# Performance work log

Measured on AMD Instinct MI355X. Metric: run time of the kernel, lower is better.

The kernel has to match this reference:

```python
import jax, jax.numpy as jnp
import numpy as np

B, M, GRID = 4, 8192, 32          # batches, points per batch, voxel grid side
N = B * M
K = 8                              # knn neighbors (includes self at dist 0)
C_IN, C_OUT, H = 8, 8, 128
KEYB = 64                          # hash base (coords shifted +1 stay in [0,33])
EPS = 1e-5


def setup_inputs() -> dict:
    rng = np.random.default_rng(0)
    # unique occupied voxels per batch (ME SparseTensor requires unique coords)
    cs = []
    for b in range(B):
        lin = rng.choice(GRID ** 3, size=M, replace=False)
        x, y, z = lin // (GRID * GRID), (lin // GRID) % GRID, lin % GRID
        cs.append(np.stack([np.full(M, b), x, y, z], axis=1))
    coords = jnp.asarray(np.concatenate(cs, axis=0).astype(np.int32))  # [N,4]

    key = jax.random.key(0)
    ks = jax.random.split(key, 4)
    feats = jax.random.normal(ks[0], (N, C_IN), jnp.float32)
    w1 = jax.random.normal(ks[1], ((K + 1) * C_IN, H), jnp.float32) * 0.05  # 1x1 conv
    g1 = jnp.ones((H,), jnp.float32)
    b1 = jnp.zeros((H,), jnp.float32)
    w3 = jax.random.normal(ks[2], (27, H, H), jnp.float32) * 0.02          # 3^3 sparse conv
    g2 = jnp.ones((H,), jnp.float32)
    b2 = jnp.zeros((H,), jnp.float32)
    w_out = jax.random.normal(ks[3], (H, 2 * C_OUT), jnp.float32) * 0.05   # 1x1 conv
    return dict(coords=coords, feats=feats, w1=w1, g1=g1, b1=b1,
                w3=w3, g2=g2, b2=b2, w_out=w_out)


def _knn_idx(coords):
    # per-batch brute-force kNN on xyz (batch column segments the search)
    xyz = coords[:, 1:].astype(jnp.float32).reshape(B, M, 3)
    d2 = jnp.sum((xyz[:, :, None, :] - xyz[:, None, :, :]) ** 2, -1)  # [B,M,M]
    _, idx = jax.lax.top_k(-d2, K)                                     # [B,M,K]
    return (idx + (jnp.arange(B) * M)[:, None, None]).reshape(N, K)


def _bn(x, g, b):
    mu = jnp.mean(x, axis=0)
    var = jnp.var(x, axis=0)
    return (x - mu) * jax.lax.rsqrt(var + EPS) * g + b


def reference(coords, feats, w1, g1, b1, w3, g2, b2, w_out):
    # --- kNN gather-and-build: [center || k neighbor feats] -> (k+1)*C_in ---
    nbr = _knn_idx(coords)                                        # [N,K] int
    combined = jnp.concatenate([feats[:, None, :], feats[nbr]], axis=1)
    combined = combined.reshape(N, (K + 1) * C_IN)
    # --- neighbor_processor: 1x1 conv + BN + ReLU ---
    h = jax.nn.relu(_bn(combined @ w1, g1, b1))                   # [N,H]
    # --- context_predictor conv k=3: gather inputs at coord+offset via hash ---
    c = coords[:, 1:] + 1                                         # shift so offsets stay >= 0
    keys = ((coords[:, 0] * KEYB + c[:, 0]) * KEYB + c[:, 1]) * KEYB + c[:, 2]
    order = jnp.argsort(keys)
    skeys = keys[order]
    offs = jnp.stack(jnp.meshgrid(*([jnp.arange(-1, 2)] * 3), indexing='ij'),
                     axis=-1).reshape(27, 3)                      # {-1,0,1}^3
    okey = (offs[:, 0] * KEYB + offs[:, 1]) * KEYB + offs[:, 2]   # [27]
    q = keys[None, :] + okey[:, None]                             # [27,N]
    pos = jnp.clip(jnp.searchsorted(skeys, q), 0, N - 1)
    valid = skeys[pos] == q                                       # [27,N]
    j = order[pos]                                                # [27,N]
    gathered = jnp.where(valid[..., None], h[j], 0.0)             # [27,N,H]
    h2 = jnp.einsum('onc,ocd->nd', gathered, w3)                  # [N,H]
    h2 = jax.nn.relu(_bn(h2, g2, b2))
    # --- final 1x1 conv -> mean/scale ---
    return h2 @ w_out                                             # [N, 2*C_OUT]
```

## Files before the change

kernel.cpp:

```cpp
#include <hip/hip_runtime.h>
#include <hip/hip_bf16.h>

#define B_   4
#define M_   8192
#define N_   32768
#define H_   128
#define EPS_ 1e-5f
#define TBL  1048576
#define GUARD 8192

typedef short short8 __attribute__((ext_vector_type(8)));
typedef float f32x4  __attribute__((ext_vector_type(4)));

__global__ __launch_bounds__(256) void prep_pack_kernel(const int* __restrict__ coords,
                                                        int* __restrict__ table,
                                                        int* __restrict__ packed,
                                                        int* __restrict__ keyb,
                                                        const float* __restrict__ w3,
                                                        ushort* __restrict__ w3f,
                                                        float* __restrict__ gsum1,
                                                        float* __restrict__ gsum2,
                                                        unsigned int* __restrict__ hbz) {
    int bid = blockIdx.x, tid = threadIdx.x;
    if (bid < 128) {
        int n = bid * 256 + tid;
        int b = coords[4*n+0], x = coords[4*n+1], y = coords[4*n+2], z = coords[4*n+3];
        packed[n] = (x << 10) | (y << 5) | z;
        int key = ((b*64 + x+1)*64 + y+1)*64 + (z+1);
        keyb[n] = key;
        table[key] = n;
        if (bid < 8)  gsum1[bid*256 + tid] = 0.f;
        if (bid == 0) gsum2[tid] = 0.f;
        if (bid == 8 && tid < 64) hbz[tid] = 0u;
        return;
    }
    int t = (bid - 128) * 256 + tid;
    int lane = t & 63;
    int ct   = (t >> 6) & 7;
    int ks   = (t >> 9) & 3;
    int o    = t >> 11;
    int quad = lane >> 4, l15 = lane & 15;
    int n = ct*16 + l15;
    const float* src = w3 + o*16384;
    ushort out8[8];
#pragma unroll
    for (int j = 0; j < 8; ++j) {
        int c = ks*32 + quad*8 + j;
        float v = src[c*128 + n];
        __hip_bfloat16 bv = __float2bfloat16(v);
        ushort u; __builtin_memcpy(&u, &bv, 2);
        out8[j] = u;
    }
    *(uint4*)&w3f[t*8] = *(uint4*)out8;
}

__global__ __launch_bounds__(256) void knn_kernel(const int* __restrict__ table,
                                                  const int* __restrict__ keyb,
                                                  const int* __restrict__ packed,
                                                  int* __restrict__ nbr) {
    __shared__ int okey_sh[96], d2_sh[96];
    __shared__ int tops[256 * 8];
    __shared__ int flagq[64];
    __shared__ int ncnt, fln;
    int tid = threadIdx.x;
    if (tid == 0) { ncnt = 0; fln = 0; }
    __syncthreads();
    if (tid < 125) {
        int dx = tid / 25 - 2, rr = tid % 25, dy = rr / 5 - 2, dz = rr % 5 - 2;
        int d2 = dx*dx + dy*dy + dz*dz;
        if (d2 <= 8) {
            int p = atomicAdd(&ncnt, 1);
            okey_sh[p] = dx * 4096 + dy * 64 + dz;
            d2_sh[p]   = d2;
        }
    }
    __syncthreads();
    if (tid < 3) { okey_sh[93 + tid] = 0; d2_sh[93 + tid] = 9; }
    __syncthreads();

    int q   = blockIdx.x * 64 + (tid >> 2);
    int sub = tid & 3;
    int kb  = keyb[q];

    int jv[24];
    int base = sub * 24;
#pragma unroll
    for (int i = 0; i < 24; ++i)
        jv[i] = table[kb + okey_sh[base + i]];

    int top[8];
#pragma unroll
    for (int k = 0; k < 8; ++k) top[k] = 0x7FFFFFFF;
#pragma unroll
    for (int i = 0; i < 24; ++i) {
        int j = jv[i];
        if (j >= 0) {
            int key = (d2_sh[base + i] << 13) | (j & 8191);
            if (key < top[7]) {
#pragma unroll
                for (int k = 7; k >= 1; --k)
                    top[k] = (key < top[k]) ? max(key, top[k-1]) : top[k];
                top[0] = min(key, top[0]);
            }
        }
    }
#pragma unroll
    for (int k = 0; k < 8; ++k) tops[tid*8 + k] = top[k];
    __syncthreads();

    if (sub == 0) {
        const int* L = &tops[tid*8];
        int ia0 = 0, ia1 = 0, ia2 = 0, ia3 = 0;
        int res[8];
#pragma unroll
        for (int k = 0; k < 8; ++k) {
            int v0 = L[ia0], v1 = L[8 + ia1], v2 = L[16 + ia2], v3 = L[24 + ia3];
            int m01 = min(v0, v1), m23 = min(v2, v3);
            int m = min(m01, m23);
            res[k] = m;
            if (m == v0) ++ia0; else if (m == v1) ++ia1;
            else if (m == v2) ++ia2; else ++ia3;
        }
        int bb = q & ~(M_-1);
        if ((res[7] >> 13) <= 8) {
#pragma unroll
            for (int k = 0; k < 8; ++k) nbr[q*8 + k] = bb + (res[k] & 8191);
        } else {
            int pos = atomicAdd(&fln, 1);
            flagq[pos] = q;
        }
    }
    __syncthreads();

    int cnt = fln;
    for (int f = 0; f < cnt; ++f) {
        int n = flagq[f];
        int bb = n & ~(M_-1);
        int p = packed[n];
        int qx = (p >> 10) & 31, qy = (p >> 5) & 31, qz = p & 31;
        int bt[8];
#pragma unroll
        for (int k = 0; k < 8; ++k) bt[k] = 0x7FFFFFFF;
        for (int j = tid; j < M_; j += 256) {
            int c = packed[bb + j];
            int dx = qx - ((c >> 10) & 31);
            int dy = qy - ((c >> 5) & 31);
            int dz = qz - (c & 31);
            int d2 = dx*dx + dy*dy + dz*dz;
            int key = (d2 << 13) | j;
            if (key < bt[7]) {
#pragma unroll
                for (int k = 7; k >= 1; --k)
                    bt[k] = (key < bt[k]) ? max(key, bt[k-1]) : bt[k];
                bt[0] = min(key, bt[0]);
            }
        }
#pragma unroll
        for (int k = 0; k < 8; ++k) tops[tid*8 + k] = bt[k];
        __syncthreads();
        for (int stride = 128; stride >= 1; stride >>= 1) {
            if (tid < stride) {
                int* A  = &tops[tid*8];
                int* Bp = &tops[(tid+stride)*8];
                int r[8]; int ia = 0, ib = 0;
#pragma unroll
                for (int k = 0; k < 8; ++k) {
                    int a = A[ia], b2 = Bp[ib];
                    if (a <= b2) { r[k] = a; ++ia; } else { r[k] = b2; ++ib; }
                }
#pragma unroll
                for (int k = 0; k < 8; ++k) A[k] = r[k];
            }
            __syncthreads();
        }
        if (tid == 0) {
#pragma unroll
            for (int k = 0; k < 8; ++k) nbr[n*8 + k] = bb + (tops[k] & 8191);
        }
        __syncthreads();
    }
}

__global__ __launch_bounds__(256) void h1_kernel(const float* __restrict__ feats,
                                                 const int* __restrict__ nbr,
                                                 const float* __restrict__ w1,
                                                 float* __restrict__ hpre,
                                                 float* __restrict__ gsum1) {
    __shared__ float comb[16][72];
    __shared__ float ssum[256], ssq[256];
    int tid = threadIdx.x;
    int rowbase = blockIdx.x * 16;
    if (tid < 144) {
        int r = tid / 9, s = tid % 9;
        int grow = rowbase + r;
        int idx = (s == 0) ? grow : nbr[grow*8 + (s-1)];
        const float4* f = (const float4*)(feats + idx * 8);
        float4 a = f[0], b = f[1];
        float* dp = &comb[r][s*8];
        dp[0]=a.x; dp[1]=a.y; dp[2]=a.z; dp[3]=a.w;
        dp[4]=b.x; dp[5]=b.y; dp[6]=b.z; dp[7]=b.w;
    }
    __syncthreads();
    int c = tid & 127, rh = tid >> 7;
    float acc[8];
#pragma unroll
    for (int i = 0; i < 8; ++i) acc[i] = 0.f;
    for (int s = 0; s < 72; ++s) {
        float w = w1[s*128 + c];
#pragma unroll
        for (int i = 0; i < 8; ++i)
            acc[i] += comb[rh*8 + i][s] * w;
    }
    float s = 0.f, q = 0.f;
#pragma unroll
    for (int i = 0; i < 8; ++i) {
        hpre[(rowbase + rh*8 + i)*128 + c] = acc[i];
        s += acc[i]; q += acc[i]*acc[i];
    }
    ssum[tid] = s; ssq[tid] = q;
    __syncthreads();
    if (tid < 128) {
        float S = ssum[tid] + ssum[tid+128];
        float Q = ssq[tid]  + ssq[tid+128];
        float* g = gsum1 + (blockIdx.x & 7) * 256;
        atomicAdd(&g[tid], S);
        atomicAdd(&g[128 + tid], Q);
    }
}

__global__ __launch_bounds__(256) void bnrelu_bf16_kernel(const float* __restrict__ x,
                                                          const float* __restrict__ gsum1,
                                                          const float* __restrict__ g1,
                                                          const float* __restrict__ b1,
                                                          ushort* __restrict__ y) {
    __shared__ float sc[128], sh[128];
    int tid = threadIdx.x;
    if (tid < 128) {
        float s = 0.f, q = 0.f;
#pragma unroll
        for (int r = 0; r < 8; ++r) {
            s += gsum1[r*256 + tid];
            q += gsum1[r*256 + 128 + tid];
        }
        float mu  = s / (float)N_;
        float var = q / (float)N_ - mu*mu;
        float inv = rsqrtf(var + EPS_);
        float scv = inv * g1[tid];
        sc[tid] = scv;
        sh[tid] = b1[tid] - mu * scv;
    }
    __syncthreads();
    int i = blockIdx.x * 256 + tid;
    float4 v = ((const float4*)x)[i];
    int c = (i * 4) & 127;
    v.x = fmaxf(0.f, v.x*sc[c]   + sh[c]);
    v.y = fmaxf(0.f, v.y*sc[c+1] + sh[c+1]);
    v.z = fmaxf(0.f, v.z*sc[c+2] + sh[c+2]);
    v.w = fmaxf(0.f, v.w*sc[c+3] + sh[c+3]);
    ushort o[4];
#pragma unroll
    for (int k = 0; k < 4; ++k) {
        float f = (&v.x)[k];
        __hip_bfloat16 bv = __float2bfloat16(f);
        __builtin_memcpy(&o[k], &bv, 2);
    }
    ((ushort4*)y)[i] = make_ushort4(o[0], o[1], o[2], o[3]);
}

#define CONV3_LDS 145408
__global__ __launch_bounds__(512) void conv3_mfma_kernel(const ushort* __restrict__ hb,
                                                         const ushort* __restrict__ w3f,
                                                         const int* __restrict__ table,
                                                         const int* __restrict__ keyb,
                                                         float* __restrict__ h2,
                                                         float* __restrict__ gsum) {
    extern __shared__ char smem_raw[];
    ushort* Asb = (ushort*)smem_raw;
    ushort* Bsb = (ushort*)(smem_raw + 65536);
    int*    jsh = (int*)(smem_raw + 131072);
    int*    kbsh= (int*)(smem_raw + 144896);

    int tid = threadIdx.x;
    int lane = tid & 63, wid = tid >> 6;
    int quad = lane >> 4, l15 = lane & 15;
    int bid = blockIdx.x;
    int swz = (bid & 7) * 32 + (bid >> 3);
    int rowbase = swz * 128;
    int wr = wid >> 1;
    int cb = (wid & 1) * 4;

    if (tid < 128) kbsh[tid] = keyb[rowbase + tid];
    __syncthreads();
    for (int t = tid; t < 27*128; t += 512) {
        int o = t >> 7, r = t & 127;
        int dx = o/9 - 1, dy = (o/3)%3 - 1, dz = o%3 - 1;
        jsh[t] = table[kbsh[r] + dx*4096 + dy*64 + dz];
    }
    __syncthreads();

#pragma unroll
    for (int i = 0; i < 4; ++i) {
        int flat = i*512 + tid;
        int r = flat >> 4, cp = flat & 15;
        int j = jsh[r];
        const ushort* asrc = hb + j*128 + ((cp ^ (r & 15)) << 3);
        __builtin_amdgcn_global_load_lds(
            (const __attribute__((address_space(1))) unsigned int*)asrc,
            (__attribute__((address_space(3))) unsigned int*)&Asb[flat << 3],
            16, 0, 0);
        __builtin_amdgcn_global_load_lds(
            (const __attribute__((address_space(1))) unsigned int*)(w3f + (flat << 3)),
            (__attribute__((address_space(3))) unsigned int*)&Bsb[flat << 3],
            16, 0, 0);
    }
    __syncthreads();

    f32x4 acc[2][4];
#pragma unroll
    for (int i = 0; i < 2; ++i)
#pragma unroll
        for (int c = 0; c < 4; ++c)
            acc[i][c] = (f32x4){0.f, 0.f, 0.f, 0.f};

    int cur = 0;
#pragma unroll 1
    for (int o = 0; o < 27; ++o) {
        if (o < 26) {
            int obase = (o + 1) << 7;
            const ushort* wsrc = w3f + ((o + 1) << 14);
            int dst = (cur ^ 1) * 16384;
#pragma unroll
            for (int i = 0; i < 4; ++i) {
                int flat = i*512 + tid;
                int r = flat >> 4, cp = flat & 15;
                int j = jsh[obase + r];
                const ushort* asrc = hb + j*128 + ((cp ^ (r & 15)) << 3);
                __builtin_amdgcn_global_load_lds(
                    (const __attribute__((address_space(1))) unsigned int*)asrc,
                    (__attribute__((address_space(3))) unsigned int*)&Asb[dst + (flat << 3)],
                    16, 0, 0);
                __builtin_amdgcn_global_load_lds(
                    (const __attribute__((address_space(1))) unsigned int*)(wsrc + (flat << 3)),
                    (__attribute__((address_space(3))) unsigned int*)&Bsb[dst + (flat << 3)],
                    16, 0, 0);
            }
        }
        const ushort* Ac = Asb + cur*16384;
        const ushort* Bc = Bsb + cur*16384;
#pragma unroll
        for (int ks = 0; ks < 4; ++ks) {
            short8 af[2], bfr[4];
#pragma unroll
            for (int i = 0; i < 2; ++i) {
                int lr = wr*32 + i*16 + l15;
                int chunk = (ks*4 + quad) ^ l15;
                af[i] = *(const short8*)&Ac[lr*128 + chunk*8];
            }
#pragma unroll
            for (int c = 0; c < 4; ++c)
                bfr[c] = *(const short8*)&Bc[((ks*8 + cb + c)*64 + lane) << 3];
#pragma unroll
            for (int i = 0; i < 2; ++i)
#pragma unroll
                for (int c = 0; c < 4; ++c)
                    acc[i][c] = __builtin_amdgcn_mfma_f32_16x16x32_bf16(af[i], bfr[c], acc[i][c], 0, 0, 0);
        }
        __syncthreads();
        cur ^= 1;
    }

    float s[4], q[4];
#pragma unroll
    for (int c = 0; c < 4; ++c) { s[c] = 0.f; q[c] = 0.f; }
#pragma unroll
    for (int i = 0; i < 2; ++i)
#pragma unroll
        for (int c = 0; c < 4; ++c)
#pragma unroll
            for (int r = 0; r < 4; ++r) {
                int row = rowbase + wr*32 + i*16 + quad*4 + r;
                int col = (cb + c)*16 + l15;
                float v = acc[i][c][r];
                h2[row*128 + col] = v;
                s[c] += v; q[c] += v*v;
            }
    float* red = (float*)smem_raw;
    if (tid < 256) red[tid] = 0.f;
    __syncthreads();
#pragma unroll
    for (int c = 0; c < 4; ++c) {
        int col = (cb + c)*16 + l15;
        atomicAdd(&red[col], s[c]);
        atomicAdd(&red[128 + col], q[c]);
    }
    __syncthreads();
    if (tid < 256) atomicAdd(&gsum[tid], red[tid]);
}

__global__ __launch_bounds__(256) void out_kernel(const float* __restrict__ h2,
                                                  const float* __restrict__ wout,
                                                  const float* __restrict__ gsum2,
                                                  const float* __restrict__ g2,
                                                  const float* __restrict__ b2,
                                                  float* __restrict__ out) {
    __shared__ float hrow[128][129];
    __shared__ float wsh[2048];
    __shared__ float sc[128], sh[128];
    int tid = threadIdx.x;
    if (tid < 128) {
        float s = gsum2[tid], q = gsum2[128 + tid];
        float mu  = s / (float)N_;
        float var = q / (float)N_ - mu*mu;
        float inv = rsqrtf(var + EPS_);
        float scv = inv * g2[tid];
        sc[tid] = scv;
        sh[tid] = b2[tid] - mu * scv;
    }
#pragma unroll
    for (int i = 0; i < 8; ++i) wsh[i*256 + tid] = wout[i*256 + tid];
    __syncthreads();

    int rowbase = blockIdx.x * 128;
#pragma unroll
    for (int i = 0; i < 16; ++i) {
        int flat = i*256 + tid;
        int row = flat >> 5, c4 = (flat & 31) * 4;
        float4 v = *(const float4*)&h2[(rowbase + row)*128 + c4];
        float4 scv = *(const float4*)&sc[c4];
        float4 shv = *(const float4*)&sh[c4];
        hrow[row][c4+0] = fmaxf(0.f, fmaf(v.x, scv.x, shv.x));
        hrow[row][c4+1] = fmaxf(0.f, fmaf(v.y, scv.y, shv.y));
        hrow[row][c4+2] = fmaxf(0.f, fmaf(v.z, scv.z, shv.z));
        hrow[row][c4+3] = fmaxf(0.f, fmaf(v.w, scv.w, shv.w));
    }
    __syncthreads();

    int row = tid >> 1, dbase = (tid & 1) * 8;
    float acc[8];
#pragma unroll
    for (int k = 0; k < 8; ++k) acc[k] = 0.f;
    for (int c = 0; c < 128; ++c) {
        float hv = hrow[row][c];
        float4 w0 = *(const float4*)&wsh[c*16 + dbase];
        float4 w1 = *(const float4*)&wsh[c*16 + dbase + 4];
        acc[0] = fmaf(hv, w0.x, acc[0]);
        acc[1] = fmaf(hv, w0.y, acc[1]);
        acc[2] = fmaf(hv, w0.z, acc[2]);
        acc[3] = fmaf(hv, w0.w, acc[3]);
        acc[4] = fmaf(hv, w1.x, acc[4]);
        acc[5] = fmaf(hv, w1.y, acc[5]);
        acc[6] = fmaf(hv, w1.z, acc[6]);
        acc[7] = fmaf(hv, w1.w, acc[7]);
    }
    float* op = out + (rowbase + row)*16 + dbase;
    *(float4*)op       = (float4){acc[0], acc[1], acc[2], acc[3]};
    *(float4*)(op + 4) = (float4){acc[4], acc[5], acc[6], acc[7]};
}

extern "C" void kernel_launch(void* const* d_in, const int* in_sizes, int n_in,
                              void* d_out, int out_size, void* d_ws, size_t ws_size,
                              hipStream_t stream) {
    const int*   coords = (const int*)d_in[0];
    const float* feats  = (const float*)d_in[1];
    const float* w1     = (const float*)d_in[2];
    const float* g1     = (const float*)d_in[3];
    const float* b1     = (const float*)d_in[4];
    const float* w3     = (const float*)d_in[5];
    const float* g2     = (const float*)d_in[6];
    const float* b2     = (const float*)d_in[7];
    const float* wout   = (const float*)d_in[8];
    float* out = (float*)d_out;

    char* ws = (char*)d_ws;
    int*    table_base = (int*)(ws);
    int*    table   = table_base + GUARD;
    int*    packed  = (int*)(ws + (4352u<<10));
    int*    keyb    = (int*)(ws + (4608u<<10));
    int*    nbr     = (int*)(ws + (4864u<<10));
    float*  gsum2   = (float*)(ws + (6416u<<10));
    float*  gsum1   = (float*)(ws + (6420u<<10));
    ushort* w3f     = (ushort*)(ws + (6656u<<10));
    ushort* hb      = (ushort*)(ws + (7680u<<10));
    float*  h       = (float*)(ws + (15872u<<10));
    float*  h2      = h;

    static bool conv3_attr_set = false;
    if (!conv3_attr_set) {
        hipFuncSetAttribute(reinterpret_cast<const void*>(&conv3_mfma_kernel),
                            hipFuncAttributeMaxDynamicSharedMemorySize, CONV3_LDS);
        conv3_attr_set = true;
    }

    hipMemsetAsync(table_base, 0xFF, (TBL + GUARD) * sizeof(int), stream);
    prep_pack_kernel <<<344, 256, 0, stream>>>(coords, table, packed, keyb, w3, w3f,
                                               gsum1, gsum2, (unsigned int*)(hb - 128));
    knn_kernel       <<<N_/64, 256, 0, stream>>>(table, keyb, packed, nbr);
    h1_kernel        <<<N_/16, 256, 0, stream>>>(feats, nbr, w1, h, gsum1);
    bnrelu_bf16_kernel<<<(N_*H_/4)/256, 256, 0, stream>>>(h, gsum1, g1, b1, hb);
    conv3_mfma_kernel<<<N_/128, 512, CONV3_LDS, stream>>>(hb, w3f, table, keyb, h2, gsum2);
    out_kernel       <<<N_/128, 256, 0, stream>>>(h2, wout, gsum2, g2, b2, out);
}
```

Before: 220.8 us.

## Fuse kNN search with first 1x1 conv, keep neighbor indices in LDS

```diff
diff --git a/kernel.cpp b/kernel.cpp
--- a/kernel.cpp
+++ b/kernel.cpp
@@ -54,14 +54,20 @@
     *(uint4*)&w3f[t*8] = *(uint4*)out8;
 }
 
-__global__ __launch_bounds__(256) void knn_kernel(const int* __restrict__ table,
-                                                  const int* __restrict__ keyb,
-                                                  const int* __restrict__ packed,
-                                                  int* __restrict__ nbr) {
-    __shared__ int okey_sh[96], d2_sh[96];
+__global__ __launch_bounds__(256) void knn_h1_kernel(const int* __restrict__ table,
+                                                     const int* __restrict__ keyb,
+                                                     const int* __restrict__ packed,
+                                                     const float* __restrict__ feats,
+                                                     const float* __restrict__ w1,
+                                                     float* __restrict__ hpre,
+                                                     float* __restrict__ gsum1) {
+    __shared__ int okey_sh[93], d2_sh[93];
     __shared__ int tops[256 * 8];
+    __shared__ int nbr_sh[64][8];
     __shared__ int flagq[64];
     __shared__ int ncnt, fln;
+    __shared__ float comb[16][72];
+    __shared__ float ssum[256], ssq[256];
     int tid = threadIdx.x;
     if (tid == 0) { ncnt = 0; fln = 0; }
     __syncthreads();
@@ -75,27 +81,23 @@
         }
     }
     __syncthreads();
-    if (tid < 3) { okey_sh[93 + tid] = 0; d2_sh[93 + tid] = 9; }
-    __syncthreads();
-
-    int q   = blockIdx.x * 64 + (tid >> 2);
-    int sub = tid & 3;
-    int kb  = keyb[q];
-
-    int jv[24];
+
+    int qloc = tid >> 2;
+    int q    = blockIdx.x * 64 + qloc;
+    int sub  = tid & 3;
+    int kb   = keyb[q];
+
+    int top[8];
+#pragma unroll
+    for (int k = 0; k < 8; ++k) top[k] = 0x7FFFFFFF;
+
     int base = sub * 24;
-#pragma unroll
-    for (int i = 0; i < 24; ++i)
-        jv[i] = table[kb + okey_sh[base + i]];
-
-    int top[8];
-#pragma unroll
-    for (int k = 0; k < 8; ++k) top[k] = 0x7FFFFFFF;
-#pragma unroll
-    for (int i = 0; i < 24; ++i) {
-        int j = jv[i];
+    int cnt  = (sub == 3) ? 21 : 24;
+    for (int i = 0; i < cnt; ++i) {
+        int idx = base + i;
+        int j = table[kb + okey_sh[idx]];
         if (j >= 0) {
-            int key = (d2_sh[base + i] << 13) | (j & 8191);
+            int key = (d2_sh[idx] << 13) | (j & 8191);
             if (key < top[7]) {
 #pragma unroll
                 for (int k = 7; k >= 1; --k)
@@ -124,17 +126,18 @@
         int bb = q & ~(M_-1);
         if ((res[7] >> 13) <= 8) {
 #pragma unroll
-            for (int k = 0; k < 8; ++k) nbr[q*8 + k] = bb + (res[k] & 8191);
+            for (int k = 0; k < 8; ++k) nbr_sh[qloc][k] = bb + (res[k] & 8191);
         } else {
             int pos = atomicAdd(&fln, 1);
-            flagq[pos] = q;
-        }
-    }
-    __syncthreads();
-
-    int cnt = fln;
-    for (int f = 0; f < cnt; ++f) {
-        int n = flagq[f];
+            flagq[pos] = qloc;
+        }
+    }
+    __syncthreads();
+
+    int fcnt = fln;
+    for (int f = 0; f < fcnt; ++f) {
+        int nloc = flagq[f];
+        int n = blockIdx.x * 64 + nloc;
         int bb = n & ~(M_-1);
         int p = packed[n];
         int qx = (p >> 10) & 31, qy = (p >> 5) & 31, qz = p & 31;
@@ -175,49 +178,44 @@
         }
         if (tid == 0) {
 #pragma unroll
-            for (int k = 0; k < 8; ++k) nbr[n*8 + k] = bb + (tops[k] & 8191);
+            for (int k = 0; k < 8; ++k) nbr_sh[nloc][k] = bb + (tops[k] & 8191);
         }
         __syncthreads();
     }
-}
-
-__global__ __launch_bounds__(256) void h1_kernel(const float* __restrict__ feats,
-                                                 const int* __restrict__ nbr,
-                                                 const float* __restrict__ w1,
-                                                 float* __restrict__ hpre,
-                                                 float* __restrict__ gsum1) {
-    __shared__ float comb[16][72];
-    __shared__ float ssum[256], ssq[256];
-    int tid = threadIdx.x;
-    int rowbase = blockIdx.x * 16;
-    if (tid < 144) {
-        int r = tid / 9, s = tid % 9;
-        int grow = rowbase + r;
-        int idx = (s == 0) ? grow : nbr[grow*8 + (s-1)];
-        const float4* f = (const float4*)(feats + idx * 8);
-        float4 a = f[0], b = f[1];
-        float* dp = &comb[r][s*8];
-        dp[0]=a.x; dp[1]=a.y; dp[2]=a.z; dp[3]=a.w;
-        dp[4]=b.x; dp[5]=b.y; dp[6]=b.z; dp[7]=b.w;
-    }
-    __syncthreads();
+
     int c = tid & 127, rh = tid >> 7;
-    float acc[8];
-#pragma unroll
-    for (int i = 0; i < 8; ++i) acc[i] = 0.f;
-    for (int s = 0; s < 72; ++s) {
-        float w = w1[s*128 + c];
-#pragma unroll
-        for (int i = 0; i < 8; ++i)
-            acc[i] += comb[rh*8 + i][s] * w;
-    }
-    float s = 0.f, q = 0.f;
-#pragma unroll
-    for (int i = 0; i < 8; ++i) {
-        hpre[(rowbase + rh*8 + i)*128 + c] = acc[i];
-        s += acc[i]; q += acc[i]*acc[i];
-    }
-    ssum[tid] = s; ssq[tid] = q;
+    float sAcc = 0.f, qAcc = 0.f;
+    for (int it = 0; it < 4; ++it) {
+        __syncthreads();
+        if (tid < 144) {
+            int r = tid / 9, s = tid % 9;
+            int rloc = it*16 + r;
+            int grow = blockIdx.x*64 + rloc;
+            int idx = (s == 0) ? grow : nbr_sh[rloc][s-1];
+            const float4* f = (const float4*)(feats + idx * 8);
+            float4 a = f[0], b = f[1];
+            float* dp = &comb[r][s*8];
+            dp[0]=a.x; dp[1]=a.y; dp[2]=a.z; dp[3]=a.w;
+            dp[4]=b.x; dp[5]=b.y; dp[6]=b.z; dp[7]=b.w;
+        }
+        __syncthreads();
+        float acc[8];
+#pragma unroll
+        for (int i = 0; i < 8; ++i) acc[i] = 0.f;
+        for (int s = 0; s < 72; ++s) {
+            float w = w1[s*128 + c];
+#pragma unroll
+            for (int i = 0; i < 8; ++i)
+                acc[i] += comb[rh*8 + i][s] * w;
+        }
+        int rowbase = blockIdx.x*64 + it*16;
+#pragma unroll
+        for (int i = 0; i < 8; ++i) {
+            hpre[(rowbase + rh*8 + i)*128 + c] = acc[i];
+            sAcc += acc[i]; qAcc += acc[i]*acc[i];
+        }
+    }
+    ssum[tid] = sAcc; ssq[tid] = qAcc;
     __syncthreads();
     if (tid < 128) {
         float S = ssum[tid] + ssum[tid+128];
@@ -476,7 +474,6 @@
     int*    table   = table_base + GUARD;
     int*    packed  = (int*)(ws + (4352u<<10));
     int*    keyb    = (int*)(ws + (4608u<<10));
-    int*    nbr     = (int*)(ws + (4864u<<10));
     float*  gsum2   = (float*)(ws + (6416u<<10));
     float*  gsum1   = (float*)(ws + (6420u<<10));
     ushort* w3f     = (ushort*)(ws + (6656u<<10));
@@ -494,8 +491,7 @@
     hipMemsetAsync(table_base, 0xFF, (TBL + GUARD) * sizeof(int), stream);
     prep_pack_kernel <<<344, 256, 0, stream>>>(coords, table, packed, keyb, w3, w3f,
                                                gsum1, gsum2, (unsigned int*)(hb - 128));
-    knn_kernel       <<<N_/64, 256, 0, stream>>>(table, keyb, packed, nbr);
-    h1_kernel        <<<N_/16, 256, 0, stream>>>(feats, nbr, w1, h, gsum1);
+    knn_h1_kernel    <<<N_/64, 256, 0, stream>>>(table, keyb, packed, feats, w1, h, gsum1);
     bnrelu_bf16_kernel<<<(N_*H_/4)/256, 256, 0, stream>>>(h, gsum1, g1, b1, hb);
     conv3_mfma_kernel<<<N_/128, 512, CONV3_LDS, stream>>>(hb, w3f, table, keyb, h2, gsum2);
     out_kernel       <<<N_/128, 256, 0, stream>>>(h2, wout, gsum2, g2, b2, out);
```

After: 219.4 us. About the same (-0.6%).
